# Kernel optimization log

Measured on AMD Instinct MI355X. Metric: run time of the kernel, lower is better.

The kernel has to match this reference:

```python
import jax, jax.numpy as jnp
import numpy as np

N_NODES = 50000
N_EDGES = 800000
IN_DIM, HID_DIM, LAT_DIM = 512, 512, 128


def _glorot(key, shape):
    fan_in = shape[0]
    return jax.random.normal(key, shape, dtype=jnp.float32) / np.sqrt(fan_in)


def setup_inputs() -> dict:
    key = jax.random.key(0)
    ks = jax.random.split(key, 10)
    x = jax.random.normal(ks[0], (N_NODES, IN_DIM), dtype=jnp.float32)
    edge_index = jax.random.randint(ks[1], (2, N_EDGES), 0, N_NODES, dtype=jnp.int64)
    edge_weight = jax.random.uniform(ks[2], (N_EDGES,), dtype=jnp.float32)
    return {
        "x": x,
        "edge_index": edge_index,
        "edge_weight": edge_weight,
        "W1": _glorot(ks[3], (IN_DIM, HID_DIM)), "b1": jnp.zeros((HID_DIM,), jnp.float32),
        "W2": _glorot(ks[4], (HID_DIM, LAT_DIM)), "b2": jnp.zeros((LAT_DIM,), jnp.float32),
        "W3": _glorot(ks[5], (LAT_DIM, HID_DIM)), "b3": jnp.zeros((HID_DIM,), jnp.float32),
        "W4": _glorot(ks[6], (HID_DIM, IN_DIM)), "b4": jnp.zeros((IN_DIM,), jnp.float32),
    }


def gcn_conv(x, W, b, src, dst, ew, n_nodes):
    """PyG GCNConv: out = D^{-1/2}(A+I)D^{-1/2} X W + b, self-loop weight 1."""
    xw = x @ W  # [N, out_dim]
    # degree over edges + self-loops (self-loop weight = 1)
    deg = jax.ops.segment_sum(ew, dst, num_segments=n_nodes) + 1.0  # [N]
    dinv = jnp.where(deg > 0, jax.lax.rsqrt(deg), 0.0)
    norm = dinv[src] * ew * dinv[dst]  # [E]
    msg = norm[:, None] * xw[src]      # [E, out_dim] per-edge gather
    agg = jax.ops.segment_sum(msg, dst, num_segments=n_nodes)  # scatter-add
    agg = agg + (dinv * dinv)[:, None] * xw  # self-loop contribution
    return agg + b


def reference(x, edge_index, edge_weight, W1, b1, W2, b2, W3, b3, W4, b4):
    src, dst = edge_index[0], edge_index[1]
    n = x.shape[0]
    # encode
    h = jax.nn.relu(gcn_conv(x, W1, b1, src, dst, edge_weight, n))
    z = gcn_conv(h, W2, b2, src, dst, edge_weight, n)
    # decode (dropout is identity in eval mode)
    h2 = jax.nn.relu(gcn_conv(z, W3, b3, src, dst, edge_weight, n))
    x_recon = gcn_conv(h2, W4, b4, src, dst, edge_weight, n)
    return (x_recon, z)
```

## Files before the change

kernel.cpp:

```cpp
#include <hip/hip_runtime.h>


typedef short bf16x8 __attribute__((ext_vector_type(8)));
typedef float f32x4 __attribute__((ext_vector_type(4)));
typedef float f32x2 __attribute__((ext_vector_type(2)));

__device__ __forceinline__ float bf2f(unsigned short u) {
  return __uint_as_float(((unsigned int)u) << 16);
}
__device__ __forceinline__ unsigned short f2bf(float f) {
  unsigned int u = __float_as_uint(f);
  return (unsigned short)((u + 0x7fffu + ((u >> 16) & 1u)) >> 16);
}

__device__ __forceinline__ void gload_lds16(const void* g, void* l) {
  __builtin_amdgcn_global_load_lds(
      (const __attribute__((address_space(1))) unsigned int*)g,
      (__attribute__((address_space(3))) unsigned int*)l, 16, 0, 0);
}


__global__ void deg_hist_kernel(const int* __restrict__ dst, const float* __restrict__ ew,
                                float* __restrict__ deg, int* __restrict__ cnt, int E) {
  int e = blockIdx.x * blockDim.x + threadIdx.x;
  if (e >= E) return;
  int d = dst[e];
  atomicAdd(&deg[d], ew[e]);
  atomicAdd(&cnt[d], 1);
}

__global__ void dinv_kernel(const float* __restrict__ deg, float* __restrict__ dinv, int n) {
  int i = blockIdx.x * blockDim.x + threadIdx.x;
  if (i >= n) return;
  dinv[i] = rsqrtf(deg[i] + 1.0f);
}

__global__ void block_sums_kernel(const int* __restrict__ cnt, int* __restrict__ sums, int n) {
  __shared__ int sh[512];
  int i = blockIdx.x * 512 + threadIdx.x;
  sh[threadIdx.x] = (i < n) ? cnt[i] : 0;
  __syncthreads();
  for (int s = 256; s > 0; s >>= 1) {
    if (threadIdx.x < s) sh[threadIdx.x] += sh[threadIdx.x + s];
    __syncthreads();
  }
  if (threadIdx.x == 0) sums[blockIdx.x] = sh[0];
}

__global__ void scan_sums_kernel(int* sums, int nb) {
  __shared__ int sh[512];
  int t = threadIdx.x;
  int v = (t < nb) ? sums[t] : 0;
  sh[t] = v;
  __syncthreads();
  for (int off = 1; off < 512; off <<= 1) {
    int y = (t >= off) ? sh[t - off] : 0;
    __syncthreads();
    sh[t] += y;
    __syncthreads();
  }
  if (t < nb) sums[t] = sh[t] - v;
}

__global__ void scan_final_kernel(const int* __restrict__ cnt, const int* __restrict__ sums,
                                  int* __restrict__ rowPtr, int* __restrict__ fill, int n) {
  __shared__ int sh[512];
  int i = blockIdx.x * 512 + threadIdx.x;
  int v = (i < n) ? cnt[i] : 0;
  sh[threadIdx.x] = v;
  __syncthreads();
  for (int off = 1; off < 512; off <<= 1) {
    int y = (threadIdx.x >= off) ? sh[threadIdx.x - off] : 0;
    __syncthreads();
    sh[threadIdx.x] += y;
    __syncthreads();
  }
  if (i < n) {
    int incl = sh[threadIdx.x];
    int base = sums[blockIdx.x];
    int excl = base + incl - v;
    rowPtr[i] = excl;
    fill[i] = excl;
    if (i == n - 1) rowPtr[n] = base + incl;
  }
}

__global__ void scatter_edges_kernel(const int* __restrict__ src, const int* __restrict__ dst,
                                     const float* __restrict__ ew, const float* __restrict__ dinv,
                                     int* __restrict__ fill, int2* __restrict__ pk, int E) {
  int e = blockIdx.x * blockDim.x + threadIdx.x;
  if (e >= E) return;
  int s = src[e], d = dst[e];
  int p = atomicAdd(&fill[d], 1);
  float v = dinv[s] * ew[e] * dinv[d];
  pk[p] = make_int2(s, __float_as_int(v));
}


__global__ void tile_w_kernel(const float* __restrict__ W, short* __restrict__ hi,
                              int K, int N) {
  int g = blockIdx.x * 256 + threadIdx.x;
  int kb_cnt = K >> 6;
  int total = (N >> 7) * kb_cnt * 1024;
  if (g >= total) return;
  int c = g & 1023;
  int t = g >> 10;
  int kb = t % kb_cnt;
  int nb = t / kb_cnt;
  int colg = (nb << 7) + (c >> 3);
  int k0 = (kb << 6) + (((c & 7) ^ ((c >> 3) & 7)) << 3);
  bf16x8 h8;
#pragma unroll
  for (int j = 0; j < 8; ++j) {
    float w = W[(size_t)(k0 + j) * N + colg];
    h8[j] = (short)f2bf(w);
  }
  *(bf16x8*)(hi + (size_t)g * 8) = h8;
}


template <int BN, bool AF32, bool BIAS, bool RELU>
__global__ __launch_bounds__(2 * BN) void mfma_gemm(
    const void* __restrict__ Aptr, const short* __restrict__ Bhi,
    const float* __restrict__ bias, unsigned short* __restrict__ C,
    int M, int N, int K) {
  constexpr int W = BN / 32;
  constexpr int RW = 128 / W;
  constexpr int IA = RW / 8;
  constexpr int NH = BN / 128;
  constexpr int WH = W / NH;
  constexpr int CW = BN / 64;

  __shared__ short As[8192];
  __shared__ short Bs[BN * 64];

  const int tid = threadIdx.x;
  const int lane = tid & 63;
  const int wave = tid >> 6;
  const int rowblk = blockIdx.y << 7;
  const int colblk = blockIdx.x * BN;
  const int wr = (wave / CW) << 6;
  const int wc = (wave % CW) << 6;
  const int lr = lane & 15;
  const int lk = lane >> 4;
  const int kbN = K >> 6;
  const int half = wave / WH;
  const int wh = wave % WH;
  const int nb0 = colblk >> 7;

  f32x4 acc[4][4];
#pragma unroll
  for (int i = 0; i < 4; ++i)
#pragma unroll
    for (int j = 0; j < 4; ++j) {
      f32x4 z = {0.f, 0.f, 0.f, 0.f};
      acc[i][j] = z;
    }

  size_t aoff[IA];
#pragma unroll
  for (int i = 0; i < IA; ++i) {
    int rg = rowblk + wave * RW + i * 8 + (lane >> 3);
    if (AF32) rg = (rg < M) ? rg : (M - 1);
    aoff[i] = (size_t)rg * K + (size_t)(((lane & 7) ^ ((lane >> 3) & 7)) << 3);
  }
  short* AsW = As + wave * (RW * 64);
  short* BsW = Bs + half * 8192 + wh * 2048;

  for (int kb = 0; kb < kbN; ++kb) {
    const short* bsrc = Bhi + ((size_t)(nb0 + half) * kbN + kb) * 8192 + (size_t)(wh * 256 + lane) * 8;
#pragma unroll
    for (int i = 0; i < 4; ++i)
      gload_lds16(bsrc + i * 512, BsW + i * 512);
#pragma unroll
    for (int i = 0; i < IA; ++i) {
      if (AF32) {
        const float* ap = (const float*)Aptr + aoff[i] + (kb << 6);
        float4 f0 = *(const float4*)ap;
        float4 f1 = *(const float4*)(ap + 4);
        bf16x8 t;
        t[0] = (short)f2bf(f0.x); t[1] = (short)f2bf(f0.y);
        t[2] = (short)f2bf(f0.z); t[3] = (short)f2bf(f0.w);
        t[4] = (short)f2bf(f1.x); t[5] = (short)f2bf(f1.y);
        t[6] = (short)f2bf(f1.z); t[7] = (short)f2bf(f1.w);
        *(bf16x8*)(AsW + i * 512 + lane * 8) = t;
      } else {
        gload_lds16((const unsigned short*)Aptr + aoff[i] + (kb << 6), AsW + i * 512);
      }
    }
    __syncthreads();
#pragma unroll
    for (int kk = 0; kk < 2; ++kk) {
      bf16x8 af[4], bhf[4];
      const int kc = kk * 4 + lk;
#pragma unroll
      for (int rb = 0; rb < 4; ++rb) {
        int rowl = wr + rb * 16 + lr;
        af[rb] = *(const bf16x8*)(As + rowl * 64 + ((kc ^ (rowl & 7)) << 3));
      }
#pragma unroll
      for (int cb = 0; cb < 4; ++cb) {
        int coll = wc + cb * 16 + lr;
        bhf[cb] = *(const bf16x8*)(Bs + coll * 64 + ((kc ^ (coll & 7)) << 3));
      }
#pragma unroll
      for (int rb = 0; rb < 4; ++rb)
#pragma unroll
        for (int cb = 0; cb < 4; ++cb)
          acc[rb][cb] = __builtin_amdgcn_mfma_f32_16x16x32_bf16(af[rb], bhf[cb], acc[rb][cb], 0, 0, 0);
    }
    __syncthreads();
  }

#pragma unroll
  for (int cb = 0; cb < 4; ++cb) {
    int colg = colblk + wc + cb * 16 + lr;
    float badd = BIAS ? bias[colg] : 0.0f;
#pragma unroll
    for (int rb = 0; rb < 4; ++rb) {
#pragma unroll
      for (int i = 0; i < 4; ++i) {
        int row = rowblk + wr + rb * 16 + lk * 4 + i;
        float v = acc[rb][cb][i] + badd;
        if (RELU) v = fmaxf(v, 0.f);
        C[(size_t)row * N + colg] = f2bf(v);
      }
    }
  }
}


template <int PT, bool INF32>
__device__ __forceinline__ void load_row(const void* p, size_t off, float* xv) {
  if (INF32) {
    if (PT == 2) {
      f32x2 f = *(const f32x2*)((const float*)p + off);
      xv[0] = f[0]; xv[1] = f[1];
    } else {
      f32x4 f0 = *(const f32x4*)((const float*)p + off);
      f32x4 f1 = *(const f32x4*)((const float*)p + off + 4);
      xv[0] = f0[0]; xv[1] = f0[1]; xv[2] = f0[2]; xv[3] = f0[3];
      xv[4] = f1[0]; xv[5] = f1[1]; xv[6] = f1[2]; xv[7] = f1[3];
    }
  } else {
    if (PT == 2) {
      unsigned int u = *(const unsigned int*)((const unsigned short*)p + off);
      xv[0] = bf2f((unsigned short)(u & 0xffffu));
      xv[1] = bf2f((unsigned short)(u >> 16));
    } else {
      bf16x8 r = *(const bf16x8*)((const short*)p + off);
#pragma unroll
      for (int j = 0; j < 8; ++j) xv[j] = bf2f((unsigned short)r[j]);
    }
  }
}

template <int PT, int UF, bool INF32, bool BIAS, bool RELU, bool W32, bool W16>
__global__ __launch_bounds__(256) void agg_kernel(
    const void* __restrict__ xw, const int2* __restrict__ pk,
    const int* __restrict__ rowPtr, const float* __restrict__ dinv,
    const float* __restrict__ bias, float* __restrict__ out32,
    unsigned short* __restrict__ out16, int n) {
  const int DIM = PT * 64;
  int node = blockIdx.x * 4 + (threadIdx.x >> 6);
  if (node >= n) return;
  int t = threadIdx.x & 63;
  float acc[PT];
#pragma unroll
  for (int q = 0; q < PT; ++q) acc[q] = 0.f;

  int beg = rowPtr[node], end = rowPtr[node + 1];
  int e = beg;
  for (; e + UF <= end; e += UF) {
    int2 p[UF];
    float xv[UF][PT];
#pragma unroll
    for (int u = 0; u < UF; ++u) p[u] = pk[e + u];
#pragma unroll
    for (int u = 0; u < UF; ++u)
      load_row<PT, INF32>(xw, (size_t)p[u].x * DIM + t * PT, xv[u]);
#pragma unroll
    for (int u = 0; u < UF; ++u) {
      float v = __int_as_float(p[u].y);
#pragma unroll
      for (int q = 0; q < PT; ++q) acc[q] += v * xv[u][q];
    }
  }
  for (; e < end; ++e) {
    int2 pe = pk[e];
    float v = __int_as_float(pe.y);
    float xv[PT];
    load_row<PT, INF32>(xw, (size_t)pe.x * DIM + t * PT, xv);
#pragma unroll
    for (int q = 0; q < PT; ++q) acc[q] += v * xv[q];
  }
  float di = dinv[node];
  float sl = di * di;
  {
    float xv[PT];
    load_row<PT, INF32>(xw, (size_t)node * DIM + t * PT, xv);
#pragma unroll
    for (int q = 0; q < PT; ++q) acc[q] += sl * xv[q];
  }
  if (BIAS) {
#pragma unroll
    for (int q = 0; q < PT; ++q) acc[q] += bias[t * PT + q];
  }
  if (RELU) {
#pragma unroll
    for (int q = 0; q < PT; ++q) acc[q] = fmaxf(acc[q], 0.f);
  }
  if (W32) {
    if (PT == 2) {
      f32x2 o;
      o[0] = acc[0]; o[1] = acc[1];
      *(f32x2*)(out32 + (size_t)node * DIM + t * PT) = o;
    } else {
      f32x4 o0, o1;
      o0[0] = acc[0]; o0[1] = acc[1]; o0[2] = acc[2]; o0[3] = acc[3];
      o1[0] = acc[4 % PT]; o1[1] = acc[5 % PT]; o1[2] = acc[6 % PT]; o1[3] = acc[7 % PT];
      *(f32x4*)(out32 + (size_t)node * DIM + t * PT) = o0;
      *(f32x4*)(out32 + (size_t)node * DIM + t * PT + 4) = o1;
    }
  }
  if (W16) {
    if (PT == 2) {
      unsigned int u = (unsigned int)f2bf(acc[0]) | ((unsigned int)f2bf(acc[1]) << 16);
      *(unsigned int*)(out16 + (size_t)node * DIM + t * PT) = u;
    } else {
      bf16x8 o;
#pragma unroll
      for (int j = 0; j < PT; ++j) o[j % 8] = (short)f2bf(acc[j]);
      *(bf16x8*)(out16 + (size_t)node * DIM + t * PT) = o;
    }
  }
}


extern "C" void kernel_launch(void* const* d_in, const int* in_sizes, int n_in,
                              void* d_out, int out_size, void* d_ws, size_t ws_size,
                              hipStream_t stream) {
  const float* x  = (const float*)d_in[0];
  const int*   ei = (const int*)d_in[1];
  const float* ew = (const float*)d_in[2];
  const float* W1 = (const float*)d_in[3];
  const float* b1 = (const float*)d_in[4];
  const float* W2 = (const float*)d_in[5];
  const float* b2 = (const float*)d_in[6];
  const float* W3 = (const float*)d_in[7];
  const float* b3 = (const float*)d_in[8];
  const float* W4 = (const float*)d_in[9];
  const float* b4 = (const float*)d_in[10];

  const int n = in_sizes[0] / 512;
  const int E = in_sizes[2];
  const int MB128 = (n + 127) / 128;
  const int Mpad = MB128 * 128;

  float* out   = (float*)d_out;
  float* z_out = out + (size_t)n * 512;

  char* w = (char*)d_ws;
  auto alloc = [&](size_t bytes) {
    char* p = w;
    w += (bytes + 255) & ~(size_t)255;
    return p;
  };
  float* deg    = (float*)alloc((size_t)n * 4);
  float* dinv   = (float*)alloc((size_t)n * 4);
  int*   cnt    = (int*)alloc((size_t)n * 4);
  int*   rowPtr = (int*)alloc((size_t)(n + 1) * 4);
  int*   fill   = (int*)alloc((size_t)n * 4);
  int*   sums   = (int*)alloc(4096);
  int2*  pk     = (int2*)alloc((size_t)E * 8);
  short* whi1 = (short*)alloc((size_t)512 * 512 * 2);
  short* whi2 = (short*)alloc((size_t)512 * 128 * 2);
  short* whi3 = (short*)alloc((size_t)128 * 512 * 2);
  short* whi4 = (short*)alloc((size_t)512 * 512 * 2);
  unsigned short* T  = (unsigned short*)alloc((size_t)Mpad * 128 * 2);
  unsigned short* B1 = (unsigned short*)alloc((size_t)Mpad * 512 * 2);
  unsigned short* B2 = (unsigned short*)alloc((size_t)Mpad * 512 * 2);

  unsigned short* zbf = B2;

  const int* srcp = ei;
  const int* dstp = ei + E;

  hipMemsetAsync(deg, 0, (size_t)n * 4, stream);
  hipMemsetAsync(cnt, 0, (size_t)n * 4, stream);
  deg_hist_kernel<<<(E + 255) / 256, 256, 0, stream>>>(dstp, ew, deg, cnt, E);
  dinv_kernel<<<(n + 255) / 256, 256, 0, stream>>>(deg, dinv, n);
  int NB = (n + 511) / 512;
  block_sums_kernel<<<NB, 512, 0, stream>>>(cnt, sums, n);
  scan_sums_kernel<<<1, 512, 0, stream>>>(sums, NB);
  scan_final_kernel<<<NB, 512, 0, stream>>>(cnt, sums, rowPtr, fill, n);
  scatter_edges_kernel<<<(E + 255) / 256, 256, 0, stream>>>(srcp, dstp, ew, dinv, fill, pk, E);

  tile_w_kernel<<<(4 * 8 * 1024 + 255) / 256, 256, 0, stream>>>(W1, whi1, 512, 512);
  tile_w_kernel<<<(1 * 8 * 1024 + 255) / 256, 256, 0, stream>>>(W2, whi2, 512, 128);
  tile_w_kernel<<<(4 * 2 * 1024 + 255) / 256, 256, 0, stream>>>(W3, whi3, 128, 512);
  tile_w_kernel<<<(4 * 8 * 1024 + 255) / 256, 256, 0, stream>>>(W4, whi4, 512, 512);

  const int AGB = (n + 3) / 4;

  mfma_gemm<512, true, false, false><<<dim3(1, MB128), 1024, 0, stream>>>(
      x, whi1, nullptr, B2, n, 512, 512);
  agg_kernel<8, 4, false, true, true, false, true><<<AGB, 256, 0, stream>>>(
      B2, pk, rowPtr, dinv, b1, nullptr, B1, n);

  mfma_gemm<128, false, false, false><<<dim3(1, MB128), 256, 0, stream>>>(
      B1, whi2, nullptr, T, Mpad, 128, 512);
  agg_kernel<2, 8, false, true, false, true, true><<<AGB, 256, 0, stream>>>(
      T, pk, rowPtr, dinv, b2, z_out, zbf, n);

  agg_kernel<2, 8, false, false, false, false, true><<<AGB, 256, 0, stream>>>(
      zbf, pk, rowPtr, dinv, nullptr, nullptr, T, n);
  mfma_gemm<512, false, true, true><<<dim3(1, MB128), 1024, 0, stream>>>(
      T, whi3, b3, B2, Mpad, 512, 128);

  mfma_gemm<512, false, false, false><<<dim3(1, MB128), 1024, 0, stream>>>(
      B2, whi4, nullptr, B1, Mpad, 512, 512);
  agg_kernel<8, 4, false, true, false, true, false><<<AGB, 256, 0, stream>>>(
      B1, pk, rowPtr, dinv, b4, out, nullptr, n);
}
```

Baseline: 625.3 us.

## Fuse small setup kernels, halve GEMM tile width, raise agg unroll

Folds the dinv computation into the block-sum kernel and merges the four weight-tiling launches into one kernel, cutting launch overhead. The 512-wide GEMMs become 256-wide tiles over two column blocks with 512 threads, which adds blocks and parallelism but reloads the A tile twice. The 128-dim aggregation kernels get a larger second template parameter (8 to 12), likely edges in flight per step.

```diff
diff --git a/kernel.cpp b/kernel.cpp
--- a/kernel.cpp
+++ b/kernel.cpp
@@ -29,16 +29,18 @@
   atomicAdd(&cnt[d], 1);
 }
 
-__global__ void dinv_kernel(const float* __restrict__ deg, float* __restrict__ dinv, int n) {
-  int i = blockIdx.x * blockDim.x + threadIdx.x;
-  if (i >= n) return;
-  dinv[i] = rsqrtf(deg[i] + 1.0f);
-}
-
-__global__ void block_sums_kernel(const int* __restrict__ cnt, int* __restrict__ sums, int n) {
+__global__ void block_sums_dinv_kernel(const int* __restrict__ cnt,
+                                       const float* __restrict__ deg,
+                                       int* __restrict__ sums,
+                                       float* __restrict__ dinv, int n) {
   __shared__ int sh[512];
   int i = blockIdx.x * 512 + threadIdx.x;
-  sh[threadIdx.x] = (i < n) ? cnt[i] : 0;
+  int v = 0;
+  if (i < n) {
+    v = cnt[i];
+    dinv[i] = rsqrtf(deg[i] + 1.0f);
+  }
+  sh[threadIdx.x] = v;
   __syncthreads();
   for (int s = 256; s > 0; s >>= 1) {
     if (threadIdx.x < s) sh[threadIdx.x] += sh[threadIdx.x + s];
@@ -97,12 +99,10 @@
 }
 
 
-__global__ void tile_w_kernel(const float* __restrict__ W, short* __restrict__ hi,
-                              int K, int N) {
-  int g = blockIdx.x * 256 + threadIdx.x;
+__device__ __forceinline__ void tile_one(const float* __restrict__ W,
+                                         short* __restrict__ hi,
+                                         int K, int N, int g) {
   int kb_cnt = K >> 6;
-  int total = (N >> 7) * kb_cnt * 1024;
-  if (g >= total) return;
   int c = g & 1023;
   int t = g >> 10;
   int kb = t % kb_cnt;
@@ -116,6 +116,17 @@
     h8[j] = (short)f2bf(w);
   }
   *(bf16x8*)(hi + (size_t)g * 8) = h8;
+}
+
+__global__ void tile_w4_kernel(const float* __restrict__ W1, short* __restrict__ h1,
+                               const float* __restrict__ W2, short* __restrict__ h2,
+                               const float* __restrict__ W3, short* __restrict__ h3,
+                               const float* __restrict__ W4, short* __restrict__ h4) {
+  int g = blockIdx.x * 256 + threadIdx.x;
+  if (g < 32768) tile_one(W1, h1, 512, 512, g);
+  else if (g < 40960) tile_one(W2, h2, 512, 128, g - 32768);
+  else if (g < 49152) tile_one(W3, h3, 128, 512, g - 40960);
+  else tile_one(W4, h4, 512, 512, g - 49152);
 }
 
 
@@ -389,36 +400,32 @@
   hipMemsetAsync(deg, 0, (size_t)n * 4, stream);
   hipMemsetAsync(cnt, 0, (size_t)n * 4, stream);
   deg_hist_kernel<<<(E + 255) / 256, 256, 0, stream>>>(dstp, ew, deg, cnt, E);
-  dinv_kernel<<<(n + 255) / 256, 256, 0, stream>>>(deg, dinv, n);
   int NB = (n + 511) / 512;
-  block_sums_kernel<<<NB, 512, 0, stream>>>(cnt, sums, n);
+  block_sums_dinv_kernel<<<NB, 512, 0, stream>>>(cnt, deg, sums, dinv, n);
   scan_sums_kernel<<<1, 512, 0, stream>>>(sums, NB);
   scan_final_kernel<<<NB, 512, 0, stream>>>(cnt, sums, rowPtr, fill, n);
   scatter_edges_kernel<<<(E + 255) / 256, 256, 0, stream>>>(srcp, dstp, ew, dinv, fill, pk, E);
 
-  tile_w_kernel<<<(4 * 8 * 1024 + 255) / 256, 256, 0, stream>>>(W1, whi1, 512, 512);
-  tile_w_kernel<<<(1 * 8 * 1024 + 255) / 256, 256, 0, stream>>>(W2, whi2, 512, 128);
-  tile_w_kernel<<<(4 * 2 * 1024 + 255) / 256, 256, 0, stream>>>(W3, whi3, 128, 512);
-  tile_w_kernel<<<(4 * 8 * 1024 + 255) / 256, 256, 0, stream>>>(W4, whi4, 512, 512);
+  tile_w4_kernel<<<320, 256, 0, stream>>>(W1, whi1, W2, whi2, W3, whi3, W4, whi4);
 
   const int AGB = (n + 3) / 4;
 
-  mfma_gemm<512, true, false, false><<<dim3(1, MB128), 1024, 0, stream>>>(
+  mfma_gemm<256, true, false, false><<<dim3(2, MB128), 512, 0, stream>>>(
       x, whi1, nullptr, B2, n, 512, 512);
   agg_kernel<8, 4, false, true, true, false, true><<<AGB, 256, 0, stream>>>(
       B2, pk, rowPtr, dinv, b1, nullptr, B1, n);
 
   mfma_gemm<128, false, false, false><<<dim3(1, MB128), 256, 0, stream>>>(
       B1, whi2, nullptr, T, Mpad, 128, 512);
-  agg_kernel<2, 8, false, true, false, true, true><<<AGB, 256, 0, stream>>>(
+  agg_kernel<2, 12, false, true, false, true, true><<<AGB, 256, 0, stream>>>(
       T, pk, rowPtr, dinv, b2, z_out, zbf, n);
 
-  agg_kernel<2, 8, false, false, false, false, true><<<AGB, 256, 0, stream>>>(
+  agg_kernel<2, 12, false, false, false, false, true><<<AGB, 256, 0, stream>>>(
       zbf, pk, rowPtr, dinv, nullptr, nullptr, T, n);
-  mfma_gemm<512, false, true, true><<<dim3(1, MB128), 1024, 0, stream>>>(
+  mfma_gemm<256, false, true, true><<<dim3(2, MB128), 512, 0, stream>>>(
       T, whi3, b3, B2, Mpad, 512, 128);
 
-  mfma_gemm<512, false, false, false><<<dim3(1, MB128), 1024, 0, stream>>>(
+  mfma_gemm<256, false, false, false><<<dim3(2, MB128), 512, 0, stream>>>(
       B2, whi4, nullptr, B1, Mpad, 512, 512);
   agg_kernel<8, 4, false, true, false, true, false><<<AGB, 256, 0, stream>>>(
       B1, pk, rowPtr, dinv, b4, out, nullptr, n);
```

New measurement: 628.6 us. About the same (+0.5%).
